# Optimization experiments

Measured on AMD Instinct MI355X. Metric: run time of the kernel, lower is better.

Reference implementation:

```python
import jax, jax.numpy as jnp
import numpy as np

B, T, N_EMBED, HEAD_SIZE = 8, 2048, 1024, 64


def setup_inputs() -> dict:
    key = jax.random.key(0)
    kx, kq, kk, kv = jax.random.split(key, 4)
    x = jax.random.normal(kx, (B, T, N_EMBED), dtype=jnp.float32)
    # nn.Linear(n_embed, head_size, bias=False) -> weight [head_size, n_embed];
    # we store the transposed [n_embed, head_size] so projection is x @ W.
    s = 1.0 / np.sqrt(N_EMBED)
    Wq = jax.random.normal(kq, (N_EMBED, HEAD_SIZE), dtype=jnp.float32) * s
    Wk = jax.random.normal(kk, (N_EMBED, HEAD_SIZE), dtype=jnp.float32) * s
    Wv = jax.random.normal(kv, (N_EMBED, HEAD_SIZE), dtype=jnp.float32) * s
    pad_mask = jnp.ones((B, T), dtype=jnp.int32)
    return {"x": x, "pad_mask": pad_mask, "Wq": Wq, "Wk": Wk, "Wv": Wv}


def reference(x, pad_mask, Wq, Wk, Wv):
    Bq, Tq, C = x.shape  # C == n_embed
    q = x @ Wq  # [B,T,H]
    k = x @ Wk  # self-attention path (enc_x is None)
    v = x @ Wv
    # NOTE: original divides by C**0.5 with C = n_embed, not head_size.
    scores = jnp.einsum("bth,bsh->bts", q, k) / jnp.sqrt(jnp.asarray(C, x.dtype))
    causal = jnp.tril(jnp.ones((Tq, Tq), dtype=bool))  # tril[:T,:T] != 0
    keep = causal[None, :, :] & (pad_mask[:, None, :] != 0)  # [B,T,T]
    scores = jnp.where(keep, scores, -jnp.inf)
    attn = jax.nn.softmax(scores, axis=-1)
    return jnp.einsum("bts,bsh->bth", attn, v)  # [B,T,head_size]
```

## Files before the change

### kernel.cpp

```cpp
#include <hip/hip_runtime.h>

#define DEV static __device__ __forceinline__

typedef float f32x4 __attribute__((ext_vector_type(4)));
typedef int i32x4 __attribute__((ext_vector_type(4)));
typedef __bf16 bf16x8 __attribute__((ext_vector_type(8)));
typedef unsigned short u16x8 __attribute__((ext_vector_type(8)));
typedef unsigned short u16x4 __attribute__((ext_vector_type(4)));

#define MFMA(a, b, c) __builtin_amdgcn_mfma_f32_16x16x32_bf16((a), (b), (c), 0, 0, 0)

#define WAIT5_BARRIER() asm volatile("s_waitcnt vmcnt(5)\n\ts_barrier" ::: "memory")
#define VM0_BARRIER()   asm volatile("s_waitcnt vmcnt(0)\n\ts_barrier" ::: "memory")
#define LGKM_BARRIER()  asm volatile("s_waitcnt lgkmcnt(0)\n\ts_barrier" ::: "memory")
#define VM_DRAIN()      asm volatile("s_waitcnt vmcnt(0)" ::: "memory")

#define TT 2048
#define CE 1024
#define HS 64

#define WBT_E 0
#define Q_E   196608
#define K_E   (Q_E + 1048576)
#define VT_E  (K_E + 1048576)
#define PO_E  (VT_E + 1048576)
#define PML_E (PO_E + 2097152)

DEV unsigned short cvt_bf16(float f) {
    unsigned int u = __builtin_bit_cast(unsigned int, f);
    u += 0x7FFFu + ((u >> 16) & 1u);
    return (unsigned short)(u >> 16);
}

DEV float bf2f(unsigned short v) {
    unsigned int u = ((unsigned int)v) << 16;
    return __builtin_bit_cast(float, u);
}

DEV bf16x8 ld_bf8(const unsigned short* p) {
    union { u16x8 u; bf16x8 b; } v;
    v.u = *(const u16x8*)p;
    return v.b;
}

DEV bf16x8 as_bf8(u16x8 u) {
    union { u16x8 u; bf16x8 b; } v;
    v.u = u;
    return v.b;
}

DEV void glds16(const void* g, void* l) {
    __builtin_amdgcn_global_load_lds(
        (const __attribute__((address_space(1))) void*)g,
        (__attribute__((address_space(3))) void*)l, 16, 0, 0);
}

__global__ __launch_bounds__(256) void wconv_kernel(
        const float* __restrict__ Wq, const float* __restrict__ Wk,
        const float* __restrict__ Wv, unsigned short* __restrict__ wbt) {
    __shared__ unsigned short Tr[64 * 72];
    const int blk = blockIdx.x;
    const int head = blk >> 4, kt = blk & 15;
    const int k0 = kt * 64;
    const float* W = (head == 0) ? Wq : ((head == 1) ? Wk : Wv);
    const float sc = (head == 0) ? 0.045084220027780106f : 1.0f;
    const int t = threadIdx.x;
    const int rrow = t >> 4, c4 = (t & 15) * 4;
    for (int i = 0; i < 4; ++i) {
        int krow = rrow + i * 16;
        f32x4 f = *(const f32x4*)(W + (size_t)(k0 + krow) * 64 + c4);
        Tr[(c4 + 0) * 72 + krow] = cvt_bf16(f[0] * sc);
        Tr[(c4 + 1) * 72 + krow] = cvt_bf16(f[1] * sc);
        Tr[(c4 + 2) * 72 + krow] = cvt_bf16(f[2] * sc);
        Tr[(c4 + 3) * 72 + krow] = cvt_bf16(f[3] * sc);
    }
    __syncthreads();
    const int n = t >> 2, off = (t & 3) * 16;
    u16x8 a0 = *(const u16x8*)&Tr[n * 72 + off];
    u16x8 a1 = *(const u16x8*)&Tr[n * 72 + off + 8];
    unsigned short* dst = wbt + head * 65536 + n * 1024 + k0 + off;
    *(u16x8*)dst = a0;
    *(u16x8*)(dst + 8) = a1;
}

__global__ __launch_bounds__(512, 2) void proj_kernel(
        const float* __restrict__ x, const unsigned short* __restrict__ wbt,
        unsigned short* __restrict__ qws, unsigned short* __restrict__ kws,
        unsigned short* __restrict__ vtws) {
    __shared__ __align__(16) float Xt0[4096], Xt1[4096], Xt2[4096];
    __shared__ __align__(16) unsigned short Wt0[12288], Wt1[12288], Wt2[12288];
    __shared__ __align__(16) unsigned short TT2[64 * 72];

    const int t = threadIdx.x;
    const int lane = t & 63, w = t >> 6;
    const int quad = lane >> 4, c = lane & 15;
    const int wm = w & 1, wn = w >> 1;
    const int t0 = blockIdx.x * 64;
    const int ck7 = c & 7;

    const int sxr = lane >> 4;
    const int sxc0 = (lane & 15) ^ sxr;
    const int sxc1 = (lane & 15) ^ ((4 + sxr) & 7);
    const float* xg0 = x + (size_t)(t0 + w * 8 + 0 + sxr) * CE + sxc0 * 4;
    const float* xg1 = x + (size_t)(t0 + w * 8 + 4 + sxr) * CE + sxc1 * 4;
    const int swc = lane >> 3;
    const int swk = (lane & 7) ^ swc;
    const unsigned short* wg0 = wbt + (size_t)(w * 24 + 0 + swc) * 1024 + swk * 8;
    const unsigned short* wg1 = wbt + (size_t)(w * 24 + 8 + swc) * 1024 + swk * 8;
    const unsigned short* wg2 = wbt + (size_t)(w * 24 + 16 + swc) * 1024 + swk * 8;

#define PSTAGE(XD, WD, ks) { \
    const int kf = (ks) * 64; \
    glds16(xg0 + kf, &XD[(w * 8 + 0) * 64]); \
    glds16(xg1 + kf, &XD[(w * 8 + 4) * 64]); \
    glds16(wg0 + kf, &WD[(w * 24 + 0) * 64]); \
    glds16(wg1 + kf, &WD[(w * 24 + 8) * 64]); \
    glds16(wg2 + kf, &WD[(w * 24 + 16) * 64]); }

    f32x4 acc[2][3] = {};

    PSTAGE(Xt0, Wt0, 0)
    PSTAGE(Xt1, Wt1, 1)

#define PITER(step, XT, WT, XD, WD) { \
    WAIT5_BARRIER(); \
    bf16x8 af[2][2]; \
    _Pragma("unroll") for (int rf = 0; rf < 2; ++rf) \
    _Pragma("unroll") for (int kk = 0; kk < 2; ++kk) { \
        const int row = wm * 32 + rf * 16 + c; \
        const int lc = kk * 8 + quad * 2; \
        f32x4 v0 = *(const f32x4*)&XT[row * 64 + ((lc ^ ck7) * 4)]; \
        f32x4 v1 = *(const f32x4*)&XT[row * 64 + (((lc + 1) ^ ck7) * 4)]; \
        u16x8 ap; \
        _Pragma("unroll") for (int j = 0; j < 4; ++j) { \
            ap[j] = cvt_bf16(v0[j]); ap[4 + j] = cvt_bf16(v1[j]); } \
        af[rf][kk] = as_bf8(ap); \
    } \
    _Pragma("unroll") for (int nt = 0; nt < 3; ++nt) \
    _Pragma("unroll") for (int kk = 0; kk < 2; ++kk) { \
        const int col = wn * 48 + nt * 16 + c; \
        bf16x8 bb = ld_bf8(&WT[col * 64 + (((kk * 4 + quad) ^ ck7) * 8)]); \
        acc[0][nt] = MFMA(af[0][kk], bb, acc[0][nt]); \
        acc[1][nt] = MFMA(af[1][kk], bb, acc[1][nt]); \
    } \
    PSTAGE(XD, WD, (((step) + 2) & 15)) }

    for (int s = 0; s < 15; s += 3) {
        PITER(s + 0, Xt0, Wt0, Xt2, Wt2)
        PITER(s + 1, Xt1, Wt1, Xt0, Wt0)
        PITER(s + 2, Xt2, Wt2, Xt1, Wt1)
    }
    PITER(15, Xt0, Wt0, Xt2, Wt2)
#undef PITER
#undef PSTAGE

#pragma unroll
    for (int rf = 0; rf < 2; ++rf) {
#pragma unroll
        for (int nt = 0; nt < 3; ++nt) {
            int col = wn * 48 + nt * 16 + c;
            f32x4 a = acc[rf][nt];
#pragma unroll
            for (int r4 = 0; r4 < 4; ++r4) {
                int row = wm * 32 + rf * 16 + quad * 4 + r4;
                size_t tg = (size_t)(t0 + row);
                unsigned short hv = cvt_bf16(a[r4]);
                if (col < 64)       qws[tg * HS + col] = hv;
                else if (col < 128) kws[tg * HS + col - 64] = hv;
                else                TT2[(col - 128) * 72 + row] = hv;
            }
        }
    }
    __syncthreads();
    {
        int h = t >> 3, off = (t & 7) * 8;
        u16x8 v = *(const u16x8*)&TT2[h * 72 + off];
        int b = t0 >> 11, tl0 = t0 & 2047;
        *(u16x8*)(vtws + (size_t)(b * 64 + h) * TT + tl0 + off) = v;
    }
}

__global__ __launch_bounds__(256) void flash_kernel(
        const unsigned short* __restrict__ qws, const unsigned short* __restrict__ kws,
        const unsigned short* __restrict__ vtws, const int* __restrict__ pmask,
        unsigned short* __restrict__ pO, float* __restrict__ pml) {
    __shared__ __align__(16) unsigned short Kt0[4096], Kt1[4096];
    __shared__ __align__(16) unsigned short Vt0[4096], Vt1[4096];
    __shared__ __align__(16) unsigned short Ps[4][1152];
    __shared__ __align__(16) float Bs[1024];

    const int t = threadIdx.x, blk = blockIdx.x;
    const int sp = blk >> 8, r8 = blk & 255, b = r8 & 7;
    int qt = r8 >> 3;
    if (sp) qt = 31 - qt;
    if (sp && qt == 0) return;
    const int half = (qt + 2) >> 1;
    const int jbeg = sp ? half : 0;
    const int jend = sp ? qt + 1 : half;
    const int niter = jend - jbeg;

    const int lane = t & 63, w = t >> 6;
    const int quad = lane >> 4, c = lane & 15;

    const int srow = lane >> 3, scb = (lane & 7) ^ srow;
    const unsigned short* kg0 = kws + (size_t)(b * TT + 2 * w * 8 + srow) * HS + scb * 8;
    const unsigned short* kg1 = kg0 + (size_t)8 * HS;
    const unsigned short* vg0 = vtws + (size_t)(b * 64 + 2 * w * 8 + srow) * TT + scb * 8;
    const unsigned short* vg1 = vg0 + (size_t)8 * TT;

#define FSTAGE(KD, VD, kv) \
    glds16(kg0 + (size_t)(kv) * HS, &KD[(2 * w + 0) * 512]); \
    glds16(kg1 + (size_t)(kv) * HS, &KD[(2 * w + 1) * 512]); \
    glds16(vg0 + (kv), &VD[(2 * w + 0) * 512]); \
    glds16(vg1 + (kv), &VD[(2 * w + 1) * 512]);

    bf16x8 qf[2];
#pragma unroll
    for (int kk = 0; kk < 2; ++kk)
        qf[kk] = ld_bf8(qws + (size_t)(b * TT + qt * 64 + w * 16 + c) * HS + kk * 32 + quad * 8);

    {
        int bi = t * 4;
        if (bi < niter * 64) {
            i32x4 pmv = *(const i32x4*)(pmask + b * TT + jbeg * 64 + bi);
            f32x4 bvv;
#pragma unroll
            for (int j = 0; j < 4; ++j) bvv[j] = pmv[j] ? 0.0f : -1e30f;
            *(f32x4*)&Bs[bi] = bvv;
        }
    }

    FSTAGE(Kt0, Vt0, jbeg * 64)
    LGKM_BARRIER();

    f32x4 o[4] = {};
    float m_run = -1e30f, l_run = 0.0f;
    const int ck7 = c & 7;

#define FITER(u, KT, VT, KD, VD) \
    if (j0 + (u) < jend) { \
        const int j = j0 + (u); \
        VM0_BARRIER(); \
        { int jn = j + 1; if (jn > jend - 1) jn = jend - 1; \
          FSTAGE(KD, VD, jn * 64) } \
        f32x4 bv[4]; \
        _Pragma("unroll") for (int nt = 0; nt < 4; ++nt) \
            bv[nt] = *(const f32x4*)&Bs[(j - jbeg) * 64 + nt * 16 + quad * 4]; \
        f32x4 s4[4] = {}; \
        _Pragma("unroll") for (int kk = 0; kk < 2; ++kk) \
        _Pragma("unroll") for (int nt = 0; nt < 4; ++nt) { \
            bf16x8 ka = ld_bf8(&KT[(nt * 16 + c) * 64 + (((kk * 4 + quad) ^ ck7) * 8)]); \
            s4[nt] = MFMA(ka, qf[kk], s4[nt]); } \
        if (j == qt) { \
            const int qrl = w * 16 + c; \
            _Pragma("unroll") for (int nt = 0; nt < 4; ++nt) \
            _Pragma("unroll") for (int r = 0; r < 4; ++r) { \
                int kvl = nt * 16 + quad * 4 + r; \
                s4[nt][r] = (kvl > qrl) ? -1e30f : (s4[nt][r] + bv[nt][r]); } \
        } else { \
            _Pragma("unroll") for (int nt = 0; nt < 4; ++nt) \
            _Pragma("unroll") for (int r = 0; r < 4; ++r) s4[nt][r] += bv[nt][r]; } \
        float mx = s4[0][0]; \
        _Pragma("unroll") for (int nt = 0; nt < 4; ++nt) \
        _Pragma("unroll") for (int r = 0; r < 4; ++r) mx = fmaxf(mx, s4[nt][r]); \
        mx = fmaxf(mx, __shfl_xor(mx, 16, 64)); \
        mx = fmaxf(mx, __shfl_xor(mx, 32, 64)); \
        float mnew = fmaxf(m_run, mx); \
        float al = exp2f(m_run - mnew); \
        m_run = mnew; \
        _Pragma("unroll") for (int nt = 0; nt < 4; ++nt) \
        _Pragma("unroll") for (int r = 0; r < 4; ++r) s4[nt][r] = exp2f(s4[nt][r] - mnew); \
        float rs = 0.0f; \
        _Pragma("unroll") for (int nt = 0; nt < 4; ++nt) \
            rs += (s4[nt][0] + s4[nt][1]) + (s4[nt][2] + s4[nt][3]); \
        rs += __shfl_xor(rs, 16, 64); \
        rs += __shfl_xor(rs, 32, 64); \
        l_run = l_run * al + rs; \
        _Pragma("unroll") for (int ht = 0; ht < 4; ++ht) \
        _Pragma("unroll") for (int r = 0; r < 4; ++r) o[ht][r] *= al; \
        _Pragma("unroll") for (int nt = 0; nt < 4; ++nt) { \
            u16x4 pk; \
            _Pragma("unroll") for (int r = 0; r < 4; ++r) pk[r] = cvt_bf16(s4[nt][r]); \
            *(u16x4*)&Ps[w][c * 72 + nt * 16 + quad * 4] = pk; } \
        bf16x8 p0 = ld_bf8(&Ps[w][c * 72 + quad * 8]); \
        bf16x8 p1 = ld_bf8(&Ps[w][c * 72 + 32 + quad * 8]); \
        _Pragma("unroll") for (int kk = 0; kk < 2; ++kk) { \
            bf16x8 pa = kk ? p1 : p0; \
            _Pragma("unroll") for (int ht = 0; ht < 4; ++ht) { \
                bf16x8 va = ld_bf8(&VT[(ht * 16 + c) * 64 + (((kk * 4 + quad) ^ ck7) * 8)]); \
                o[ht] = MFMA(va, pa, o[ht]); } } \
    }

    for (int j0 = jbeg; j0 < jend; j0 += 2) {
        FITER(0, Kt0, Vt0, Kt1, Vt1)
        FITER(1, Kt1, Vt1, Kt0, Vt0)
    }
#undef FITER
#undef FSTAGE

    VM_DRAIN();

    unsigned short* po = pO + (size_t)blk * 4096;
#pragma unroll
    for (int ht = 0; ht < 4; ++ht) {
        u16x4 pk;
#pragma unroll
        for (int r = 0; r < 4; ++r) pk[r] = cvt_bf16(o[ht][r]);
        *(u16x4*)(po + (w * 16 + c) * 64 + ht * 16 + quad * 4) = pk;
    }
    if (quad == 0) {
        pml[(size_t)blk * 128 + (w * 16 + c) * 2] = m_run;
        pml[(size_t)blk * 128 + (w * 16 + c) * 2 + 1] = l_run;
    }
}

__global__ __launch_bounds__(256) void combine_kernel(
        const unsigned short* __restrict__ pO, const float* __restrict__ pml,
        float* __restrict__ out) {
    const int blk = blockIdx.x;
    const int qt = blk >> 3, b = blk & 7;
    const int s0 = qt * 8 + b, s1 = 256 + (31 - qt) * 8 + b;
    const bool two = (qt > 0);
    const int t = threadIdx.x, h = t & 63, rg = t >> 6;
    for (int i = 0; i < 16; ++i) {
        int row = rg + i * 4;
        float m0 = pml[(size_t)s0 * 128 + row * 2];
        float l0 = pml[(size_t)s0 * 128 + row * 2 + 1];
        float o0 = bf2f(pO[(size_t)s0 * 4096 + row * 64 + h]);
        float num, den;
        if (two) {
            float m1 = pml[(size_t)s1 * 128 + row * 2];
            float l1 = pml[(size_t)s1 * 128 + row * 2 + 1];
            float o1 = bf2f(pO[(size_t)s1 * 4096 + row * 64 + h]);
            float M = fmaxf(m0, m1);
            float w0 = exp2f(m0 - M), w1 = exp2f(m1 - M);
            num = o0 * w0 + o1 * w1;
            den = l0 * w0 + l1 * w1;
        } else {
            num = o0; den = l0;
        }
        out[(size_t)(b * TT + qt * 64 + row) * HS + h] = num / den;
    }
}

extern "C" void kernel_launch(void* const* d_in, const int* in_sizes, int n_in,
                              void* d_out, int out_size, void* d_ws, size_t ws_size,
                              hipStream_t stream) {
    const float* x  = (const float*)d_in[0];
    const int* pm   = (const int*)d_in[1];
    const float* Wq = (const float*)d_in[2];
    const float* Wk = (const float*)d_in[3];
    const float* Wv = (const float*)d_in[4];
    float* out = (float*)d_out;

    unsigned short* wsu  = (unsigned short*)d_ws;
    unsigned short* wbt  = wsu + WBT_E;
    unsigned short* qws  = wsu + Q_E;
    unsigned short* kws  = wsu + K_E;
    unsigned short* vtws = wsu + VT_E;
    unsigned short* pO   = wsu + PO_E;
    float* pml           = (float*)(wsu + PML_E);

    wconv_kernel<<<48, 256, 0, stream>>>(Wq, Wk, Wv, wbt);
    proj_kernel<<<256, 512, 0, stream>>>(x, wbt, qws, kws, vtws);
    flash_kernel<<<512, 256, 0, stream>>>(qws, kws, vtws, pm, pO, pml);
    combine_kernel<<<256, 256, 0, stream>>>(pO, pml, out);
}
```

Baseline: 149.0 us.

## Split causal KV range into fixed 4-tile chunks across more blocks

Replaces the two-way split-K of each query tile with a split into chunks of at most four KV tiles. This yields 144 work items per batch, 1152 blocks in total, each with bounded work. The combine kernel now merges a variable number of partials per query tile using log-sum-exp rescaling. The aim is better load balance and occupancy on the causal triangle. The cost is more partial-output traffic, a larger workspace, and more combine work. Shared memory is also trimmed by shrinking Bs.

```diff
diff --git a/kernel.cpp b/kernel.cpp
--- a/kernel.cpp
+++ b/kernel.cpp
@@ -24,7 +24,7 @@
 #define K_E   (Q_E + 1048576)
 #define VT_E  (K_E + 1048576)
 #define PO_E  (VT_E + 1048576)
-#define PML_E (PO_E + 2097152)
+#define PML_E (PO_E + 4718592)
 
 DEV unsigned short cvt_bf16(float f) {
     unsigned int u = __builtin_bit_cast(unsigned int, f);
@@ -187,16 +187,19 @@
     __shared__ __align__(16) unsigned short Kt0[4096], Kt1[4096];
     __shared__ __align__(16) unsigned short Vt0[4096], Vt1[4096];
     __shared__ __align__(16) unsigned short Ps[4][1152];
-    __shared__ __align__(16) float Bs[1024];
+    __shared__ __align__(16) float Bs[256];
 
     const int t = threadIdx.x, blk = blockIdx.x;
-    const int sp = blk >> 8, r8 = blk & 255, b = r8 & 7;
-    int qt = r8 >> 3;
-    if (sp) qt = 31 - qt;
-    if (sp && qt == 0) return;
-    const int half = (qt + 2) >> 1;
-    const int jbeg = sp ? half : 0;
-    const int jend = sp ? qt + 1 : half;
+    const int b = blk / 144, cid = blk - b * 144;
+    int g = 0;
+    while (cid >= 2 * (g + 1) * (g + 2)) ++g;
+    const int off = cid - 2 * g * (g + 1);
+    const int qi = off / (g + 1);
+    const int chunk = off - qi * (g + 1);
+    const int qt = 4 * g + qi;
+    const int jbeg = chunk * 4;
+    int je = jbeg + 4; if (je > qt + 1) je = qt + 1;
+    const int jend = je;
     const int niter = jend - jbeg;
 
     const int lane = t & 63, w = t >> 6;
@@ -319,25 +322,23 @@
         float* __restrict__ out) {
     const int blk = blockIdx.x;
     const int qt = blk >> 3, b = blk & 7;
-    const int s0 = qt * 8 + b, s1 = 256 + (31 - qt) * 8 + b;
-    const bool two = (qt > 0);
+    const int g = qt >> 2;
+    const int nc = g + 1;
+    const int s0 = b * 144 + 2 * g * (g + 1) + (qt - 4 * g) * (g + 1);
     const int t = threadIdx.x, h = t & 63, rg = t >> 6;
     for (int i = 0; i < 16; ++i) {
         int row = rg + i * 4;
-        float m0 = pml[(size_t)s0 * 128 + row * 2];
-        float l0 = pml[(size_t)s0 * 128 + row * 2 + 1];
-        float o0 = bf2f(pO[(size_t)s0 * 4096 + row * 64 + h]);
-        float num, den;
-        if (two) {
-            float m1 = pml[(size_t)s1 * 128 + row * 2];
-            float l1 = pml[(size_t)s1 * 128 + row * 2 + 1];
-            float o1 = bf2f(pO[(size_t)s1 * 4096 + row * 64 + h]);
-            float M = fmaxf(m0, m1);
-            float w0 = exp2f(m0 - M), w1 = exp2f(m1 - M);
-            num = o0 * w0 + o1 * w1;
-            den = l0 * w0 + l1 * w1;
-        } else {
-            num = o0; den = l0;
+        float M = -3e38f;
+        for (int s = 0; s < nc; ++s)
+            M = fmaxf(M, pml[(size_t)(s0 + s) * 128 + row * 2]);
+        float num = 0.0f, den = 0.0f;
+        for (int s = 0; s < nc; ++s) {
+            float m = pml[(size_t)(s0 + s) * 128 + row * 2];
+            float l = pml[(size_t)(s0 + s) * 128 + row * 2 + 1];
+            float ov = bf2f(pO[(size_t)(s0 + s) * 4096 + row * 64 + h]);
+            float ww = exp2f(m - M);
+            num += ov * ww;
+            den += l * ww;
         }
         out[(size_t)(b * TT + qt * 64 + row) * HS + h] = num / den;
     }
@@ -363,6 +364,6 @@
 
     wconv_kernel<<<48, 256, 0, stream>>>(Wq, Wk, Wv, wbt);
     proj_kernel<<<256, 512, 0, stream>>>(x, wbt, qws, kws, vtws);
-    flash_kernel<<<512, 256, 0, stream>>>(qws, kws, vtws, pm, pO, pml);
+    flash_kernel<<<1152, 256, 0, stream>>>(qws, kws, vtws, pm, pO, pml);
     combine_kernel<<<256, 256, 0, stream>>>(pO, pml, out);
 }
```

Result: slower. 184.5 us (+23.8%).
